# Performance work log

Hardware: AMD Instinct MI355X
Metric: run time of the kernel (lower is better)

The kernel has to match this reference:

```python
import jax, jax.numpy as jnp
import numpy as np

DIM = 1024
NUM_HEADS = 16
HEAD_DIM = DIM // NUM_HEADS


def setup_inputs() -> dict:
    key = jax.random.key(0)
    k_x, k_q, k_k, k_v, k_o = jax.random.split(key, 5)
    B, L = 2, 2048
    scale = 1.0 / np.sqrt(DIM)
    x_bld = jax.random.normal(k_x, (B, L, DIM), dtype=jnp.float32)
    # LinearGeneral kernels: (in_features, num_heads, head_dim) for q/k/v,
    # (num_heads, head_dim, out_features) for out. Init ~ lecun_normal-ish scale.
    Wq = jax.random.normal(k_q, (DIM, NUM_HEADS, HEAD_DIM), dtype=jnp.float32) * scale
    Wk = jax.random.normal(k_k, (DIM, NUM_HEADS, HEAD_DIM), dtype=jnp.float32) * scale
    Wv = jax.random.normal(k_v, (DIM, NUM_HEADS, HEAD_DIM), dtype=jnp.float32) * scale
    Wo = jax.random.normal(k_o, (NUM_HEADS, HEAD_DIM, DIM), dtype=jnp.float32) * scale
    return {"x_bld": x_bld, "Wq": Wq, "Wk": Wk, "Wv": Wv, "Wo": Wo}


def reference(x_bld, Wq, Wk, Wv, Wo) -> jnp.ndarray:
    # Projections: [B,L,D] x [D,H,hd] -> [B,L,H,hd]
    q_blhd = jnp.einsum('bld,dhk->blhk', x_bld, Wq)
    k_blhd = jnp.einsum('bld,dhk->blhk', x_bld, Wk)
    v_blhd = jnp.einsum('bld,dhk->blhk', x_bld, Wv)
    # Scores: [B,H,L,L]
    attn_bhll = jnp.einsum('bqhd,bkhd->bhqk', q_blhd, k_blhd)
    attn_bhll = attn_bhll / jnp.sqrt(jnp.asarray(HEAD_DIM, dtype=attn_bhll.dtype))
    L = x_bld.shape[1]
    qi = jnp.arange(L)[:, None]
    ki = jnp.arange(L)[None, :]
    mask_ll = ki <= qi  # causal, no window
    neg_inf = jnp.finfo(attn_bhll.dtype).min
    attn_bhll = jnp.where(mask_ll[None, None, :, :], attn_bhll, neg_inf)
    attn_bhll = jax.nn.softmax(attn_bhll, axis=-1)
    y_blhd = jnp.einsum('bhqk,bkhd->bqhd', attn_bhll, v_blhd)
    # Output projection: contract (H, hd) -> D
    return jnp.einsum('blhk,hkd->bld', y_blhd, Wo)
```

## Files before the change

### kernel.cpp

```cpp
#include <hip/hip_runtime.h>
#include <hip/hip_bf16.h>

typedef __hip_bfloat16 bf16;
typedef __attribute__((ext_vector_type(8))) short short8;
typedef __attribute__((ext_vector_type(4))) float f32x4;
typedef __attribute__((ext_vector_type(4))) unsigned int u32x4;

__device__ __forceinline__ float bfbits2f(unsigned short u) {
    return __uint_as_float(((unsigned int)u) << 16);
}
__device__ __forceinline__ unsigned short f2bfbits(float f) {
    union { float f; unsigned int u; } x;
    x.f = f;
    unsigned int r = x.u + 0x7FFFu + ((x.u >> 16) & 1u);
    return (unsigned short)(r >> 16);
}
__device__ __forceinline__ unsigned int pack_bf16x2(float lo, float hi) {
    unsigned int u0 = __float_as_uint(lo) + 0x8000u;
    unsigned int u1 = __float_as_uint(hi) + 0x8000u;
    return __builtin_amdgcn_perm(u1, u0, 0x07060302u);
}
__device__ __forceinline__ void async_copy16(const void* g, void* l) {
    __builtin_amdgcn_global_load_lds(
        (const __attribute__((address_space(1))) void*)g,
        (__attribute__((address_space(3))) void*)l, 16, 0, 0);
}
__device__ __forceinline__ bool sniff_bf16(const unsigned int* p, int lane) {
    unsigned int wd = p[lane];
    unsigned int e = (wd >> 7) & 0xFFu;
    return __popcll(__ballot(e >= 90u && e <= 150u)) > 40;
}

__global__ __launch_bounds__(256) void prep(
    const void* __restrict__ X, const void* __restrict__ W1,
    const void* __restrict__ W2, const void* __restrict__ W3,
    const void* __restrict__ W4, short* __restrict__ xb,
    short* __restrict__ O1, short* __restrict__ O2,
    short* __restrict__ O3, short* __restrict__ O4) {
    __shared__ float tbuf[32][33];
    const int bx = blockIdx.x;
    const int tid = threadIdx.x;
    const int lane = tid & 63;

    if (bx < 2048) {
        const bool isBf = sniff_bf16((const unsigned int*)X, lane);
        const int i = (bx * 256 + tid) * 8;
        if (isBf) {
            *(short8*)&xb[i] = *(const short8*)((const short*)X + i);
        } else {
            const float* xf = (const float*)X + i;
            float4 a = *(const float4*)xf;
            float4 b = *(const float4*)(xf + 4);
            short8 o;
            o[0] = (short)f2bfbits(a.x); o[1] = (short)f2bfbits(a.y);
            o[2] = (short)f2bfbits(a.z); o[3] = (short)f2bfbits(a.w);
            o[4] = (short)f2bfbits(b.x); o[5] = (short)f2bfbits(b.y);
            o[6] = (short)f2bfbits(b.z); o[7] = (short)f2bfbits(b.w);
            *(short8*)&xb[i] = o;
        }
    } else {
        const void* Ws[4] = {W1, W2, W3, W4};
        short* Os[4] = {O1, O2, O3, O4};
        const int t = bx - 2048;
        const int wsel = t >> 10;
        const int tile = t & 1023;
        const int bxt = tile & 31, byt = tile >> 5;
        const void* W = Ws[wsel];
        const bool isBf = sniff_bf16((const unsigned int*)W, lane);
        const float scale = (wsel == 0) ? 0.18033688f : 1.0f;
        short* O = Os[wsel];

        const int tx = tid & 31, ty = tid >> 5;
        const int gx = bxt * 32 + tx;
#pragma unroll
        for (int i = 0; i < 4; i++) {
            const int gy = byt * 32 + ty + i * 8;
            float v = isBf
                ? bfbits2f(((const unsigned short*)W)[(size_t)gy * 1024 + gx])
                : ((const float*)W)[(size_t)gy * 1024 + gx];
            tbuf[ty + i * 8][tx] = v * scale;
        }
        __syncthreads();
#pragma unroll
        for (int i = 0; i < 4; i++) {
            const int orow = bxt * 32 + ty + i * 8;
            const int ocol = byt * 32 + tx;
            O[(size_t)orow * 1024 + ocol] = (short)f2bfbits(tbuf[tx][ty + i * 8]);
        }
    }
}

__global__ __launch_bounds__(256) void transpose_v(const short* __restrict__ qkv,
                                                   short* __restrict__ VtG) {
    __shared__ short t[32][33];
    const int tx = threadIdx.x & 31, ty = threadIdx.x >> 5;
    const int b = blockIdx.z >> 4, h = blockIdx.z & 15;
    const int l0 = blockIdx.x * 32, d0 = blockIdx.y * 32;
#pragma unroll
    for (int i = 0; i < 4; i++) {
        const int l = l0 + ty + i * 8;
        t[ty + i * 8][tx] =
            qkv[(size_t)(b * 2048 + l) * 3072 + 2048 + h * 64 + d0 + tx];
    }
    __syncthreads();
    const int ptx = 2 * (tx & 15) + (tx >> 4);
#pragma unroll
    for (int i = 0; i < 4; i++) {
        const int d = d0 + ty + i * 8;
        VtG[((size_t)(b * 16 + h) * 64 + d) * 2048 + l0 + ptx] = t[tx][ty + i * 8];
    }
}

template <int BN>
__global__ __launch_bounds__(256) void gemm_async(const short* __restrict__ A,
                                                  const short* __restrict__ Bt,
                                                  void* __restrict__ C,
                                                  const unsigned int* __restrict__ xdet,
                                                  int M, int N, int K) {
    __shared__ short As[2][128 * 32];
    __shared__ short Bs[2][BN * 32];
    constexpr int NI = BN / 32;

    const int tid = threadIdx.x;
    const int lane = tid & 63;
    const int wv = __builtin_amdgcn_readfirstlane(tid >> 6);
    const int quad = lane >> 4, l16 = lane & 15;
    const int wr = wv >> 1, wc = wv & 1;
    const int m0 = blockIdx.y * 128, n0 = blockIdx.x * BN;

    const int gr = lane >> 2;
    const int gc = ((lane & 3) ^ ((lane >> 3) & 3)) * 8;

    const f32x4 zero = {0.f, 0.f, 0.f, 0.f};
    f32x4 acc[4][NI];
#pragma unroll
    for (int mi = 0; mi < 4; mi++)
#pragma unroll
        for (int ni = 0; ni < NI; ni++) acc[mi][ni] = zero;

    const short* aptr[2];
    const short* bptr[BN / 64];
#pragma unroll
    for (int t = 0; t < 2; t++)
        aptr[t] = A + (size_t)(m0 + t * 64 + wv * 16 + gr) * K + gc;
#pragma unroll
    for (int t = 0; t < BN / 64; t++)
        bptr[t] = Bt + (size_t)(n0 + t * 64 + wv * 16 + gr) * K + gc;

#pragma unroll
    for (int t = 0; t < 2; t++) async_copy16(aptr[t], &As[0][(t * 64 + wv * 16) * 32]);
#pragma unroll
    for (int t = 0; t < BN / 64; t++) async_copy16(bptr[t], &Bs[0][(t * 64 + wv * 16) * 32]);

    const int ss = (quad ^ ((l16 >> 1) & 3)) * 8;

    for (int k0 = 0; k0 < K; k0 += 32) {
        const int cur = (k0 >> 5) & 1;
        __syncthreads();
        if (k0 + 32 < K) {
            const int nxt = cur ^ 1;
#pragma unroll
            for (int t = 0; t < 2; t++)
                async_copy16(aptr[t] + k0 + 32, &As[nxt][(t * 64 + wv * 16) * 32]);
#pragma unroll
            for (int t = 0; t < BN / 64; t++)
                async_copy16(bptr[t] + k0 + 32, &Bs[nxt][(t * 64 + wv * 16) * 32]);
        }

        short8 af[4], bfv[NI];
#pragma unroll
        for (int mi = 0; mi < 4; mi++)
            af[mi] = *(const short8*)&As[cur][(wr * 64 + mi * 16 + l16) * 32 + ss];
#pragma unroll
        for (int ni = 0; ni < NI; ni++)
            bfv[ni] = *(const short8*)&Bs[cur][(wc * (BN / 2) + ni * 16 + l16) * 32 + ss];
#pragma unroll
        for (int mi = 0; mi < 4; mi++)
#pragma unroll
            for (int ni = 0; ni < NI; ni++)
                acc[mi][ni] = __builtin_amdgcn_mfma_f32_16x16x32_bf16(
                    af[mi], bfv[ni], acc[mi][ni], 0, 0, 0);
    }

    bool outBf = true;
    if (xdet) outBf = sniff_bf16(xdet, lane);
    if (outBf) {
        unsigned short* Cb = (unsigned short*)C;
#pragma unroll
        for (int mi = 0; mi < 4; mi++)
#pragma unroll
            for (int ni = 0; ni < NI; ni++)
#pragma unroll
                for (int r = 0; r < 4; r++) {
                    const int row = m0 + wr * 64 + mi * 16 + quad * 4 + r;
                    const int col = n0 + wc * (BN / 2) + ni * 16 + l16;
                    Cb[(size_t)row * N + col] = f2bfbits(acc[mi][ni][r]);
                }
    } else {
        float* Cf = (float*)C;
#pragma unroll
        for (int mi = 0; mi < 4; mi++)
#pragma unroll
            for (int ni = 0; ni < NI; ni++)
#pragma unroll
                for (int r = 0; r < 4; r++) {
                    const int row = m0 + wr * 64 + mi * 16 + quad * 4 + r;
                    const int col = n0 + wc * (BN / 2) + ni * 16 + l16;
                    Cf[(size_t)row * N + col] = acc[mi][ni][r];
                }
    }
}

__global__ __launch_bounds__(256) void attn_mfma10(
    const short* __restrict__ qkv, const short* __restrict__ VtG,
    short* __restrict__ Yg, short* __restrict__ Opart, float* __restrict__ ml) {
    __shared__ short KV[3][2][64 * 64];
    __shared__ float lred[2][64];

    const int tid = threadIdx.x;
    const int lane = tid & 63;
    const int wv = __builtin_amdgcn_readfirstlane(tid >> 6);
    const int wvq = wv >> 1, wvk = wv & 1;
    const int quad = lane >> 4, l16 = lane & 15;
    const int bh = blockIdx.x;
    const int b = bh >> 4, h = bh & 15;

    int qb, seg, S;
    const int slot = blockIdx.y;
    if (slot < 64)      { qb = 31 - (slot >> 2); seg = slot & 3; S = 4; }
    else if (slot < 80) { const int t2 = slot - 64; qb = 15 - (t2 >> 1); seg = t2 & 1; S = 2; }
    else                { qb = 87 - slot; seg = 0; S = 1; }

    const int ns = qb + 1;
    const int sb0 = seg * ns / S;
    const int sb1 = (seg + 1) * ns / S;

    const int rr = lane >> 3;
    const int scol = ((lane & 7) ^ rr) * 8;

    const short* kptr[2];
    const short* vptr[2];
    short* kdst[2];
    short* vdst[2];
#pragma unroll
    for (int i = 0; i < 2; i++) {
        const int u = wv * 2 + i;
        kptr[i] = qkv + (size_t)(b * 2048 + sb0 * 64 + u * 8 + rr) * 3072 + 1024 +
                  h * 64 + scol;
        kdst[i] = &KV[0][0][(u * 8) * 64];
        vptr[i] = VtG + ((size_t)bh * 64 + u * 8 + rr) * 2048 + sb0 * 64 + scol;
        vdst[i] = &KV[0][1][(u * 8) * 64];
    }

    short8 qf[2][2];
    {
        const short* qbase = qkv + (size_t)(b * 2048 + qb * 64 + wvq * 32 + l16) * 3072 +
                             h * 64 + quad * 8;
#pragma unroll
        for (int qt = 0; qt < 2; qt++)
#pragma unroll
            for (int hf = 0; hf < 2; hf++)
                qf[qt][hf] = *(const short8*)(qbase + qt * 16 * 3072 + hf * 32);
    }
    asm volatile("s_waitcnt vmcnt(0)" ::: "memory");

    constexpr int BUFS = 2 * 64 * 64;
    auto STAGE = [&](int bufi) {
#pragma unroll
        for (int i = 0; i < 2; i++) {
            async_copy16(kptr[i], kdst[i] + bufi * BUFS);
            async_copy16(vptr[i], vdst[i] + bufi * BUFS);
            kptr[i] += 64 * 3072;
            vptr[i] += 64;
        }
    };
    STAGE(0);
    if (sb0 + 1 < sb1) STAGE(1);

    const int sl = (quad ^ (l16 & 7)) * 8;

    const f32x4 minit = {-17.3123405f, -17.3123405f, -17.3123405f, -17.3123405f};
    const short8 vone = {(short)0x3F80, (short)0x3F80, (short)0x3F80, (short)0x3F80,
                         (short)0x3F80, (short)0x3F80, (short)0x3F80, (short)0x3F80};
    f32x4 O[2][4];
#pragma unroll
    for (int qt = 0; qt < 2; qt++)
#pragma unroll
        for (int dt = 0; dt < 4; dt++) O[qt][dt] = {0.f, 0.f, 0.f, 0.f};
    f32x4 lacc[2] = {{0.f, 0.f, 0.f, 0.f}, {0.f, 0.f, 0.f, 0.f}};
    const int keyA0 = wvk * 32 + quad * 4;

    int cb = 0;
    for (int sb = sb0; sb < sb1; sb++) {
        if (sb + 1 < sb1) asm volatile("s_waitcnt vmcnt(4)" ::: "memory");
        else              asm volatile("s_waitcnt vmcnt(0)" ::: "memory");
        __builtin_amdgcn_s_barrier();
        asm volatile("" ::: "memory");
        if (sb + 2 < sb1) {
            int st = cb + 2; if (st >= 3) st -= 3;
            STAGE(st);
        }
        const short* Kc = &KV[cb][0][0];
        const short* Vc = &KV[cb][1][0];

        short8 kf[2][2], vf[4];
#pragma unroll
        for (int kt = 0; kt < 2; kt++)
#pragma unroll
            for (int hf = 0; hf < 2; hf++)
                kf[kt][hf] = *(const short8*)
                    &Kc[(wvk * 32 + kt * 16 + l16) * 64 + (sl ^ (hf << 5))];
#pragma unroll
        for (int dt = 0; dt < 4; dt++)
            vf[dt] = *(const short8*)
                &Vc[(dt * 16 + l16) * 64 + (sl ^ (wvk << 5))];

#pragma unroll
        for (int qt = 0; qt < 2; qt++) {
            f32x4 sA = __builtin_amdgcn_mfma_f32_16x16x32_bf16(kf[0][0], qf[qt][0], minit, 0, 0, 0);
            sA = __builtin_amdgcn_mfma_f32_16x16x32_bf16(kf[0][1], qf[qt][1], sA, 0, 0, 0);
            f32x4 sB = __builtin_amdgcn_mfma_f32_16x16x32_bf16(kf[1][0], qf[qt][0], minit, 0, 0, 0);
            sB = __builtin_amdgcn_mfma_f32_16x16x32_bf16(kf[1][1], qf[qt][1], sB, 0, 0, 0);
            if (sb == qb) {
                const int qcol = wvq * 32 + qt * 16 + l16;
#pragma unroll
                for (int r = 0; r < 4; r++) {
                    if (keyA0 + r > qcol) sA[r] = -1e30f;
                    if (keyA0 + 16 + r > qcol) sB[r] = -1e30f;
                }
            }
            union { u32x4 u; short8 s; } pa;
#pragma unroll
            for (int t = 0; t < 4; t++) {
                sA[t] = __builtin_amdgcn_exp2f(sA[t]);
                sB[t] = __builtin_amdgcn_exp2f(sB[t]);
                pa.u[t] = pack_bf16x2(sA[t], sB[t]);
            }
            __builtin_amdgcn_s_setprio(1);
#pragma unroll
            for (int dt = 0; dt < 4; dt++)
                O[qt][dt] = __builtin_amdgcn_mfma_f32_16x16x32_bf16(
                    pa.s, vf[dt], O[qt][dt], 0, 0, 0);
            lacc[qt] = __builtin_amdgcn_mfma_f32_16x16x32_bf16(
                pa.s, vone, lacc[qt], 0, 0, 0);
            __builtin_amdgcn_s_setprio(0);
        }
        cb++; if (cb == 3) cb = 0;
    }

    if (l16 == 0) {
#pragma unroll
        for (int qt = 0; qt < 2; qt++)
#pragma unroll
            for (int r = 0; r < 4; r++)
                lred[wvk][wvq * 32 + qt * 16 + quad * 4 + r] = lacc[qt][r];
    }

    __syncthreads();
    float* scrf = (float*)&KV[0][0][0];
    if (wvk == 1) {
#pragma unroll
        for (int qt = 0; qt < 2; qt++)
#pragma unroll
            for (int dt = 0; dt < 4; dt++)
#pragma unroll
                for (int r = 0; r < 4; r++)
                    scrf[(wvq * 32 + qt * 16 + quad * 4 + r) * 68 + dt * 16 + l16] =
                        O[qt][dt][r];
    }
    __syncthreads();

    if (wvk == 0) {
#pragma unroll
        for (int qt = 0; qt < 2; qt++)
#pragma unroll
            for (int dt = 0; dt < 4; dt++)
#pragma unroll
                for (int r = 0; r < 4; r++)
                    O[qt][dt][r] += scrf[(wvq * 32 + qt * 16 + quad * 4 + r) * 68 +
                                         dt * 16 + l16];
        if (S == 1) {
#pragma unroll
            for (int qt = 0; qt < 2; qt++)
#pragma unroll
                for (int r = 0; r < 4; r++) {
                    const int q = wvq * 32 + qt * 16 + quad * 4 + r;
                    const float inv = 1.f / (lred[0][q] + lred[1][q]);
#pragma unroll
                    for (int dt = 0; dt < 4; dt++)
                        Yg[(size_t)(b * 2048 + qb * 64 + q) * 1024 + h * 64 +
                           dt * 16 + l16] = (short)f2bfbits(O[qt][dt][r] * inv);
                }
        } else {
            const int qidx = qb - 8;
            const int base = ((seg * 32 + bh) * 24 + qidx) * 64;
#pragma unroll
            for (int qt = 0; qt < 2; qt++)
#pragma unroll
                for (int r = 0; r < 4; r++) {
                    const int q = wvq * 32 + qt * 16 + quad * 4 + r;
#pragma unroll
                    for (int dt = 0; dt < 4; dt++)
                        Opart[(size_t)(base + q) * 64 + dt * 16 + l16] =
                            (short)f2bfbits(O[qt][dt][r]);
                    if (l16 == 0) ml[base + q] = lred[0][q] + lred[1][q];
                }
        }
    }
}

__global__ __launch_bounds__(256) void attn_combine6(
    const short* __restrict__ Opart, const float* __restrict__ ml,
    short* __restrict__ Yg) {
    const int qb = 8 + blockIdx.x;
    const int bh = blockIdx.y;
    const int b = bh >> 4, h = bh & 15;
    const int S = (qb >= 16) ? 4 : 2;
    const int qidx = qb - 8;
    const int tid = threadIdx.x;
    const int q = tid >> 2;
    const int d0 = (tid & 3) * 16;

    float a0[8] = {}, a1[8] = {};
    float lsum = 0.f;
    for (int s = 0; s < S; s++) {
        const int idx = ((s * 32 + bh) * 24 + qidx) * 64 + q;
        lsum += ml[idx];
        const short* p = Opart + (size_t)idx * 64 + d0;
        short8 x0 = *(const short8*)p;
        short8 x1 = *(const short8*)(p + 8);
#pragma unroll
        for (int t = 0; t < 8; t++) {
            a0[t] += bfbits2f((unsigned short)x0[t]);
            a1[t] += bfbits2f((unsigned short)x1[t]);
        }
    }
    const float inv = 1.f / lsum;
    short8 o0, o1;
#pragma unroll
    for (int t = 0; t < 8; t++) {
        o0[t] = (short)f2bfbits(a0[t] * inv);
        o1[t] = (short)f2bfbits(a1[t] * inv);
    }
    short* yp = Yg + (size_t)(b * 2048 + qb * 64 + q) * 1024 + h * 64 + d0;
    *(short8*)yp = o0;
    *(short8*)(yp + 8) = o1;
}

extern "C" void kernel_launch(void* const* d_in, const int* in_sizes, int n_in,
                              void* d_out, int out_size, void* d_ws, size_t ws_size,
                              hipStream_t stream) {
    const int M = 2 * 2048;
    const int D = 1024;

    char* w = (char*)d_ws;
    short* xb  = (short*)w;
    short* WqT = (short*)(w + (8u << 20));
    short* WkT = WqT + (1u << 20);
    short* WvT = WkT + (1u << 20);
    short* WoT = WvT + (1u << 20);
    short* qkv = WoT + (1u << 20);
    short* VtG = qkv + (size_t)M * 3072;
    short* Opart = VtG + (size_t)2048 * 2048;
    float* mlp = (float*)(Opart + (size_t)4 * 32 * 24 * 64 * 64);
    short* y = xb;

    prep<<<6144, 256, 0, stream>>>(d_in[0], d_in[1], d_in[2], d_in[3], d_in[4],
                                   xb, WqT, WkT, WvT, WoT);

    gemm_async<128><<<dim3(3072 / 128, M / 128), 256, 0, stream>>>(
        xb, WqT, qkv, nullptr, M, 3072, D);

    transpose_v<<<dim3(64, 2, 32), 256, 0, stream>>>(qkv, VtG);

    attn_mfma10<<<dim3(32, 88), 256, 0, stream>>>(qkv, VtG, y, Opart, mlp);
    attn_combine6<<<dim3(24, 32), 256, 0, stream>>>(Opart, mlp, y);

    gemm_async<64><<<dim3(D / 64, M / 128), 256, 0, stream>>>(
        y, WoT, d_out, (const unsigned int*)d_in[0], M, D, D);
}
```

Baseline: 186.6 us.

## Use 128-row query tiles with 512-thread attention blocks and double-buffered KV

The attention kernel now handles 128 query rows per block with 8 waves instead of 64 rows with 4 waves, so every K/V tile loaded into LDS serves twice as many queries. K and V staging is split across wave groups, and the triple buffer is replaced by a double buffer with a plain __syncthreads, with masking computed per tile. The bf16 packing switches to the hardware v_cvt_pk_bf16_f32 instruction, and the split-combine indexing is updated to the new tile size. In exchange the grid has half as many blocks, which may hurt load balance, and the shallower prefetch depth may expose more memory latency.

```diff
diff --git a/kernel.cpp b/kernel.cpp
--- a/kernel.cpp
+++ b/kernel.cpp
@@ -15,10 +15,10 @@
     unsigned int r = x.u + 0x7FFFu + ((x.u >> 16) & 1u);
     return (unsigned short)(r >> 16);
 }
-__device__ __forceinline__ unsigned int pack_bf16x2(float lo, float hi) {
-    unsigned int u0 = __float_as_uint(lo) + 0x8000u;
-    unsigned int u1 = __float_as_uint(hi) + 0x8000u;
-    return __builtin_amdgcn_perm(u1, u0, 0x07060302u);
+__device__ __forceinline__ unsigned int cvtpk_bf16x2(float lo, float hi) {
+    unsigned int w;
+    asm("v_cvt_pk_bf16_f32 %0, %1, %2" : "=v"(w) : "v"(lo), "v"(hi));
+    return w;
 }
 __device__ __forceinline__ void async_copy16(const void* g, void* l) {
     __builtin_amdgcn_global_load_lds(
@@ -211,11 +211,13 @@
     }
 }
 
-__global__ __launch_bounds__(256) void attn_mfma10(
+__global__ __launch_bounds__(512, 6) void attn_mfma11(
     const short* __restrict__ qkv, const short* __restrict__ VtG,
     short* __restrict__ Yg, short* __restrict__ Opart, float* __restrict__ ml) {
-    __shared__ short KV[3][2][64 * 64];
-    __shared__ float lred[2][64];
+    __shared__ char smem[34816 + 1024];
+    short* KVs = (short*)smem;
+    float* scrf = (float*)smem;
+    float* lred = (float*)(smem + 34816);
 
     const int tid = threadIdx.x;
     const int lane = tid & 63;
@@ -225,57 +227,57 @@
     const int bh = blockIdx.x;
     const int b = bh >> 4, h = bh & 15;
 
-    int qb, seg, S;
+    int qbb, seg, S;
     const int slot = blockIdx.y;
-    if (slot < 64)      { qb = 31 - (slot >> 2); seg = slot & 3; S = 4; }
-    else if (slot < 80) { const int t2 = slot - 64; qb = 15 - (t2 >> 1); seg = t2 & 1; S = 2; }
-    else                { qb = 87 - slot; seg = 0; S = 1; }
-
-    const int ns = qb + 1;
+    if (slot < 32)      { qbb = 15 - (slot >> 2); seg = slot & 3; S = 4; }
+    else if (slot < 40) { const int t2 = slot - 32; qbb = 7 - (t2 >> 1); seg = t2 & 1; S = 2; }
+    else                { qbb = 43 - slot; seg = 0; S = 1; }
+
+    const int ns = 2 * qbb + 2;
     const int sb0 = seg * ns / S;
     const int sb1 = (seg + 1) * ns / S;
 
     const int rr = lane >> 3;
     const int scol = ((lane & 7) ^ rr) * 8;
-
-    const short* kptr[2];
-    const short* vptr[2];
-    short* kdst[2];
-    short* vdst[2];
+    const bool stK = (wv < 4);
+    const int su = (wv & 3) * 2;
+
+    const short* sptr[2];
+    short* sdst[2];
 #pragma unroll
     for (int i = 0; i < 2; i++) {
-        const int u = wv * 2 + i;
-        kptr[i] = qkv + (size_t)(b * 2048 + sb0 * 64 + u * 8 + rr) * 3072 + 1024 +
-                  h * 64 + scol;
-        kdst[i] = &KV[0][0][(u * 8) * 64];
-        vptr[i] = VtG + ((size_t)bh * 64 + u * 8 + rr) * 2048 + sb0 * 64 + scol;
-        vdst[i] = &KV[0][1][(u * 8) * 64];
-    }
+        const int u = su + i;
+        if (stK) {
+            sptr[i] = qkv + (size_t)(b * 2048 + sb0 * 64 + u * 8 + rr) * 3072 + 1024 +
+                      h * 64 + scol;
+            sdst[i] = KVs + (u * 8) * 64;
+        } else {
+            sptr[i] = VtG + ((size_t)bh * 64 + u * 8 + rr) * 2048 + sb0 * 64 + scol;
+            sdst[i] = KVs + 4096 + (u * 8) * 64;
+        }
+    }
+    const size_t sadv = stK ? (size_t)64 * 3072 : (size_t)64;
+
+    constexpr int BUFS = 2 * 64 * 64;
+    auto STAGE = [&](int bufi) {
+#pragma unroll
+        for (int i = 0; i < 2; i++) {
+            async_copy16(sptr[i], sdst[i] + bufi * BUFS);
+            sptr[i] += sadv;
+        }
+    };
+    STAGE(0);
 
     short8 qf[2][2];
     {
-        const short* qbase = qkv + (size_t)(b * 2048 + qb * 64 + wvq * 32 + l16) * 3072 +
-                             h * 64 + quad * 8;
+        const short* qbase = qkv +
+            (size_t)(b * 2048 + qbb * 128 + wvq * 32 + l16) * 3072 + h * 64 + quad * 8;
 #pragma unroll
         for (int qt = 0; qt < 2; qt++)
 #pragma unroll
             for (int hf = 0; hf < 2; hf++)
                 qf[qt][hf] = *(const short8*)(qbase + qt * 16 * 3072 + hf * 32);
     }
-    asm volatile("s_waitcnt vmcnt(0)" ::: "memory");
-
-    constexpr int BUFS = 2 * 64 * 64;
-    auto STAGE = [&](int bufi) {
-#pragma unroll
-        for (int i = 0; i < 2; i++) {
-            async_copy16(kptr[i], kdst[i] + bufi * BUFS);
-            async_copy16(vptr[i], vdst[i] + bufi * BUFS);
-            kptr[i] += 64 * 3072;
-            vptr[i] += 64;
-        }
-    };
-    STAGE(0);
-    if (sb0 + 1 < sb1) STAGE(1);
 
     const int sl = (quad ^ (l16 & 7)) * 8;
 
@@ -288,20 +290,15 @@
 #pragma unroll
         for (int dt = 0; dt < 4; dt++) O[qt][dt] = {0.f, 0.f, 0.f, 0.f};
     f32x4 lacc[2] = {{0.f, 0.f, 0.f, 0.f}, {0.f, 0.f, 0.f, 0.f}};
-    const int keyA0 = wvk * 32 + quad * 4;
-
-    int cb = 0;
-    for (int sb = sb0; sb < sb1; sb++) {
-        if (sb + 1 < sb1) asm volatile("s_waitcnt vmcnt(4)" ::: "memory");
-        else              asm volatile("s_waitcnt vmcnt(0)" ::: "memory");
-        __builtin_amdgcn_s_barrier();
-        asm volatile("" ::: "memory");
-        if (sb + 2 < sb1) {
-            int st = cb + 2; if (st >= 3) st -= 3;
-            STAGE(st);
-        }
-        const short* Kc = &KV[cb][0][0];
-        const short* Vc = &KV[cb][1][0];
+
+    const int qmin = qbb * 128 + wvq * 32;
+    const int keyoff = wvk * 32 + quad * 4;
+
+    auto STEP = [&](int sb, int cur, bool pf) {
+        __syncthreads();
+        if (pf) STAGE(cur ^ 1);
+        const short* Kc = KVs + cur * BUFS;
+        const short* Vc = KVs + cur * BUFS + 4096;
 
         short8 kf[2][2], vf[4];
 #pragma unroll
@@ -315,18 +312,20 @@
             vf[dt] = *(const short8*)
                 &Vc[(dt * 16 + l16) * 64 + (sl ^ (wvk << 5))];
 
+        const bool needmask = (sb * 64 + 63 > qmin);
 #pragma unroll
         for (int qt = 0; qt < 2; qt++) {
             f32x4 sA = __builtin_amdgcn_mfma_f32_16x16x32_bf16(kf[0][0], qf[qt][0], minit, 0, 0, 0);
             sA = __builtin_amdgcn_mfma_f32_16x16x32_bf16(kf[0][1], qf[qt][1], sA, 0, 0, 0);
             f32x4 sB = __builtin_amdgcn_mfma_f32_16x16x32_bf16(kf[1][0], qf[qt][0], minit, 0, 0, 0);
             sB = __builtin_amdgcn_mfma_f32_16x16x32_bf16(kf[1][1], qf[qt][1], sB, 0, 0, 0);
-            if (sb == qb) {
-                const int qcol = wvq * 32 + qt * 16 + l16;
+            if (needmask) {
+                const int qcol = qmin + qt * 16 + l16;
+                const int key0 = sb * 64 + keyoff;
 #pragma unroll
                 for (int r = 0; r < 4; r++) {
-                    if (keyA0 + r > qcol) sA[r] = -1e30f;
-                    if (keyA0 + 16 + r > qcol) sB[r] = -1e30f;
+                    if (key0 + r > qcol) sA[r] = -1e30f;
+                    if (key0 + 16 + r > qcol) sB[r] = -1e30f;
                 }
             }
             union { u32x4 u; short8 s; } pa;
@@ -334,7 +333,7 @@
             for (int t = 0; t < 4; t++) {
                 sA[t] = __builtin_amdgcn_exp2f(sA[t]);
                 sB[t] = __builtin_amdgcn_exp2f(sB[t]);
-                pa.u[t] = pack_bf16x2(sA[t], sB[t]);
+                pa.u[t] = cvtpk_bf16x2(sA[t], sB[t]);
             }
             __builtin_amdgcn_s_setprio(1);
 #pragma unroll
@@ -345,19 +344,25 @@
                 pa.s, vone, lacc[qt], 0, 0, 0);
             __builtin_amdgcn_s_setprio(0);
         }
-        cb++; if (cb == 3) cb = 0;
-    }
+    };
+
+    const int n = sb1 - sb0;
+    int i = 0;
+    for (; i + 2 <= n; i += 2) {
+        STEP(sb0 + i, 0, true);
+        STEP(sb0 + i + 1, 1, i + 2 < n);
+    }
+    if (i < n) STEP(sb0 + i, 0, false);
 
     if (l16 == 0) {
 #pragma unroll
         for (int qt = 0; qt < 2; qt++)
 #pragma unroll
             for (int r = 0; r < 4; r++)
-                lred[wvk][wvq * 32 + qt * 16 + quad * 4 + r] = lacc[qt][r];
+                lred[wvk * 128 + wvq * 32 + qt * 16 + quad * 4 + r] = lacc[qt][r];
     }
 
     __syncthreads();
-    float* scrf = (float*)&KV[0][0][0];
     if (wvk == 1) {
 #pragma unroll
         for (int qt = 0; qt < 2; qt++)
@@ -385,15 +390,15 @@
 #pragma unroll
                 for (int r = 0; r < 4; r++) {
                     const int q = wvq * 32 + qt * 16 + quad * 4 + r;
-                    const float inv = 1.f / (lred[0][q] + lred[1][q]);
+                    const float inv = 1.f / (lred[q] + lred[128 + q]);
 #pragma unroll
                     for (int dt = 0; dt < 4; dt++)
-                        Yg[(size_t)(b * 2048 + qb * 64 + q) * 1024 + h * 64 +
+                        Yg[(size_t)(b * 2048 + qbb * 128 + q) * 1024 + h * 64 +
                            dt * 16 + l16] = (short)f2bfbits(O[qt][dt][r] * inv);
                 }
         } else {
-            const int qidx = qb - 8;
-            const int base = ((seg * 32 + bh) * 24 + qidx) * 64;
+            const int qidx = qbb - 4;
+            const int base = ((seg * 32 + bh) * 12 + qidx) * 128;
 #pragma unroll
             for (int qt = 0; qt < 2; qt++)
 #pragma unroll
@@ -403,28 +408,30 @@
                     for (int dt = 0; dt < 4; dt++)
                         Opart[(size_t)(base + q) * 64 + dt * 16 + l16] =
                             (short)f2bfbits(O[qt][dt][r]);
-                    if (l16 == 0) ml[base + q] = lred[0][q] + lred[1][q];
+                    if (l16 == 0) ml[base + q] = lred[q] + lred[128 + q];
                 }
         }
     }
 }
 
-__global__ __launch_bounds__(256) void attn_combine6(
+__global__ __launch_bounds__(256) void attn_combine11(
     const short* __restrict__ Opart, const float* __restrict__ ml,
     short* __restrict__ Yg) {
-    const int qb = 8 + blockIdx.x;
+    const int x = blockIdx.x;
+    const int qbb = 4 + (x >> 1);
+    const int half = x & 1;
     const int bh = blockIdx.y;
     const int b = bh >> 4, h = bh & 15;
-    const int S = (qb >= 16) ? 4 : 2;
-    const int qidx = qb - 8;
+    const int S = (qbb >= 8) ? 4 : 2;
+    const int qidx = qbb - 4;
     const int tid = threadIdx.x;
-    const int q = tid >> 2;
+    const int q = (tid >> 2) + half * 64;
     const int d0 = (tid & 3) * 16;
 
     float a0[8] = {}, a1[8] = {};
     float lsum = 0.f;
     for (int s = 0; s < S; s++) {
-        const int idx = ((s * 32 + bh) * 24 + qidx) * 64 + q;
+        const int idx = ((s * 32 + bh) * 12 + qidx) * 128 + q;
         lsum += ml[idx];
         const short* p = Opart + (size_t)idx * 64 + d0;
         short8 x0 = *(const short8*)p;
@@ -442,7 +449,7 @@
         o0[t] = (short)f2bfbits(a0[t] * inv);
         o1[t] = (short)f2bfbits(a1[t] * inv);
     }
-    short* yp = Yg + (size_t)(b * 2048 + qb * 64 + q) * 1024 + h * 64 + d0;
+    short* yp = Yg + (size_t)(b * 2048 + qbb * 128 + q) * 1024 + h * 64 + d0;
     *(short8*)yp = o0;
     *(short8*)(yp + 8) = o1;
 }
@@ -462,7 +469,7 @@
     short* qkv = WoT + (1u << 20);
     short* VtG = qkv + (size_t)M * 3072;
     short* Opart = VtG + (size_t)2048 * 2048;
-    float* mlp = (float*)(Opart + (size_t)4 * 32 * 24 * 64 * 64);
+    float* mlp = (float*)(Opart + (size_t)4 * 32 * 12 * 128 * 64);
     short* y = xb;
 
     prep<<<6144, 256, 0, stream>>>(d_in[0], d_in[1], d_in[2], d_in[3], d_in[4],
@@ -473,8 +480,8 @@
 
     transpose_v<<<dim3(64, 2, 32), 256, 0, stream>>>(qkv, VtG);
 
-    attn_mfma10<<<dim3(32, 88), 256, 0, stream>>>(qkv, VtG, y, Opart, mlp);
-    attn_combine6<<<dim3(24, 32), 256, 0, stream>>>(Opart, mlp, y);
+    attn_mfma11<<<dim3(32, 44), 512, 0, stream>>>(qkv, VtG, y, Opart, mlp);
+    attn_combine11<<<dim3(24, 32), 256, 0, stream>>>(Opart, mlp, y);
 
     gemm_async<64><<<dim3(D / 64, M / 128), 256, 0, stream>>>(
         y, WoT, d_out, (const unsigned int*)d_in[0], M, D, D);
```

Result: slower. 390.2 us (+109.1%).
